# Kernel tuning notes

Measured on AMD Instinct MI355X. Metric: run time of the kernel, lower is better.

## Reference

```python
import jax, jax.numpy as jnp
import numpy as np

NUM_CLASSES = 81
THRESH_HI = 0.5
THRESH_LO = 0.4
GAMMA = 2.0
ALPHA = 0.25
VARIANCE = (0.1, 0.2)  # cfg['variance'] in ssd.pytorch
B, P, T = 32, 24564, 20


def setup_inputs() -> dict:
    key = jax.random.key(0)
    k1, k2, k3, k4, k5, k6, k7 = jax.random.split(key, 7)
    loc_data = jax.random.normal(k1, (B, P, 4), jnp.float32)
    conf_data = jax.random.normal(k2, (B, P, NUM_CLASSES), jnp.float32)
    # priors in center form (cx, cy, w, h), all in [0,1]
    pcxy = jax.random.uniform(k3, (P, 2), minval=0.05, maxval=0.95)
    pwh = jax.random.uniform(k4, (P, 2), minval=0.04, maxval=0.5)
    priors = jnp.concatenate([pcxy, pwh], axis=-1).astype(jnp.float32)
    # ground-truth boxes in point form (xmin, ymin, xmax, ymax) + label
    tcxy = jax.random.uniform(k5, (B, T, 2), minval=0.1, maxval=0.9)
    twh = jax.random.uniform(k6, (B, T, 2), minval=0.05, maxval=0.4)
    boxes = jnp.clip(jnp.concatenate([tcxy - twh / 2, tcxy + twh / 2], -1), 0.0, 1.0)
    labels = jax.random.randint(k7, (B, T), 0, NUM_CLASSES - 1).astype(jnp.float32)
    targets = jnp.concatenate([boxes, labels[..., None]], axis=-1)  # [B,T,5]
    return {"loc_data": loc_data, "conf_data": conf_data, "priors": priors, "targets": targets}


def point_form(pr):
    # center form -> (xmin,ymin,xmax,ymax)
    return jnp.concatenate([pr[:, :2] - pr[:, 2:] / 2, pr[:, :2] + pr[:, 2:] / 2], -1)


def jaccard(box_a, box_b):
    # box_a [T,4], box_b [P,4], both point form -> IoU [T,P]
    lt = jnp.maximum(box_a[:, None, :2], box_b[None, :, :2])
    rb = jnp.minimum(box_a[:, None, 2:], box_b[None, :, 2:])
    wh = jnp.clip(rb - lt, 0.0)
    inter = wh[..., 0] * wh[..., 1]
    area_a = ((box_a[:, 2] - box_a[:, 0]) * (box_a[:, 3] - box_a[:, 1]))[:, None]
    area_b = ((box_b[:, 2] - box_b[:, 0]) * (box_b[:, 3] - box_b[:, 1]))[None, :]
    return inter / (area_a + area_b - inter)


def encode(matched, priors):
    # matched [P,4] point form, priors [P,4] center form
    g_cxcy = ((matched[:, :2] + matched[:, 2:]) / 2 - priors[:, :2]) / (VARIANCE[0] * priors[:, 2:])
    g_wh = jnp.log((matched[:, 2:] - matched[:, :2]) / priors[:, 2:]) / VARIANCE[1]
    return jnp.concatenate([g_cxcy, g_wh], -1)


def match_one(truths, labels, priors):
    # truths [T,4] point form, labels [T], priors [P,4] center form
    ov = jaccard(truths, point_form(priors))          # [T,P]
    best_prior_idx = jnp.argmax(ov, axis=1)           # [T] best prior per gt
    best_truth_overlap = jnp.max(ov, axis=0)          # [P]
    best_truth_idx = jnp.argmax(ov, axis=0)           # [P]
    # ensure every gt box keeps its best prior
    best_truth_overlap = best_truth_overlap.at[best_prior_idx].set(2.0)
    best_truth_idx = best_truth_idx.at[best_prior_idx].set(jnp.arange(truths.shape[0]))
    matched = truths[best_truth_idx]                  # [P,4]
    conf = labels[best_truth_idx].astype(jnp.int32) + 1
    conf = jnp.where(best_truth_overlap < THRESH_HI, -1, conf)  # ignore band
    conf = jnp.where(best_truth_overlap < THRESH_LO, 0, conf)   # background
    return encode(matched, priors), conf


def reference(loc_data, conf_data, priors, targets):
    truths = targets[..., :4]
    labels = targets[..., 4]
    loc_t, conf_t = jax.vmap(lambda t, l: match_one(t, l, priors))(truths, labels)
    pos = conf_t > 0                                  # [B,P]
    # smooth L1 over positive priors (sum reduction)
    diff = loc_data - loc_t
    ad = jnp.abs(diff)
    sl1 = jnp.where(ad < 1.0, 0.5 * diff * diff, ad - 0.5)
    loss_l = jnp.sum(sl1 * pos[..., None])
    # focal loss over ALL locations (ignore conf==-1)
    logits = conf_data.reshape(-1, NUM_CLASSES)
    tgt = conf_t.reshape(-1)
    valid = tgt >= 0
    tgt_safe = jnp.where(valid, tgt, 0)
    logpt = jnp.take_along_axis(jax.nn.log_softmax(logits, -1), tgt_safe[:, None], 1)[:, 0]
    pt = jnp.exp(logpt)
    alpha_t = jnp.where(tgt > 0, ALPHA, 1.0 - ALPHA)
    fl = -alpha_t * (1.0 - pt) ** GAMMA * logpt
    loss_c = jnp.sum(jnp.where(valid, fl, 0.0))
    n = jnp.sum(pos).astype(loc_data.dtype)
    return loss_l / n, loss_c / n
```

## Files before the change

### kernel.cpp

```cpp
#include <hip/hip_runtime.h>

#define NCLS 81
#define BB 32
#define PP 24564
#define TT 20
#define BP_SEGS 8
#define BP_SEG 3072
#define KL_BLOCKS 1024
#define KL_ROWS 32
#define KL_CHUNKS ((BB * PP) / KL_ROWS)
#define KL_F4 ((KL_ROWS * NCLS) / 4)

#define GLOAD_LDS16(g, l)                                                  \
    __builtin_amdgcn_global_load_lds(                                      \
        (const __attribute__((address_space(1))) void*)(g),                \
        (__attribute__((address_space(3))) void*)(l), 16, 0, 0)

__global__ __launch_bounds__(1024)
void k_bp(const float* __restrict__ priors,
          const float* __restrict__ targets,
          unsigned long long* __restrict__ bp_part,
          unsigned long long* __restrict__ bovbt)
{
    const int seg = blockIdx.x;
    const int b = blockIdx.y;

    __shared__ float trb[TT * 5];
    __shared__ unsigned long long wred[TT][16];
    if (threadIdx.x < TT * 5) trb[threadIdx.x] = targets[b * TT * 5 + threadIdx.x];
    __syncthreads();

    float X1[3], Y1[3], X2[3], Y2[3], pa[3];
    unsigned int pkey[3];
    bool ok[3];
    #pragma unroll
    for (int j = 0; j < 3; ++j) {
        int p = seg * BP_SEG + j * 1024 + threadIdx.x;
        ok[j] = p < PP;
        float4 pr = ok[j] ? ((const float4*)priors)[p] : make_float4(1.f, 1.f, 0.f, 0.f);
        float hw = __fmul_rn(pr.z, 0.5f), hh = __fmul_rn(pr.w, 0.5f);
        X1[j] = __fsub_rn(pr.x, hw); Y1[j] = __fsub_rn(pr.y, hh);
        X2[j] = __fadd_rn(pr.x, hw); Y2[j] = __fadd_rn(pr.y, hh);
        pa[j] = __fmul_rn(__fsub_rn(X2[j], X1[j]), __fsub_rn(Y2[j], Y1[j]));
        pkey[j] = 0xFFFFFFFFu - (unsigned)p;
    }

    const int wv = threadIdx.x >> 6;
    const int lane = threadIdx.x & 63;

    unsigned long long bkey[3] = {0ull, 0ull, 0ull};

    for (int t = 0; t < TT; ++t) {
        float tx1 = trb[t * 5 + 0], ty1 = trb[t * 5 + 1];
        float tx2 = trb[t * 5 + 2], ty2 = trb[t * 5 + 3];
        float ta = __fmul_rn(__fsub_rn(tx2, tx1), __fsub_rn(ty2, ty1));

        unsigned long long best = 0ull;
        #pragma unroll
        for (int j = 0; j < 3; ++j) {
            float lx = fmaxf(tx1, X1[j]), ly = fmaxf(ty1, Y1[j]);
            float rx = fminf(tx2, X2[j]), ry = fminf(ty2, Y2[j]);
            float w = fmaxf(__fsub_rn(rx, lx), 0.0f);
            float h = fmaxf(__fsub_rn(ry, ly), 0.0f);
            float inter = __fmul_rn(w, h);
            float denom = __fsub_rn(__fadd_rn(ta, pa[j]), inter);
            float ov = __fdiv_rn(inter, denom);
            unsigned long long ovhi = (unsigned long long)__float_as_uint(ov) << 32;
            unsigned long long key = ok[j] ? (ovhi | pkey[j]) : 0ull;
            if (key > best) best = key;
            unsigned long long rowk = ovhi | (unsigned long long)(31 - t);
            if (rowk > bkey[j]) bkey[j] = rowk;
        }
        #pragma unroll
        for (int s = 32; s; s >>= 1) {
            unsigned long long o = __shfl_xor(best, s, 64);
            if (o > best) best = o;
        }
        if (lane == 0) wred[t][wv] = best;
    }

    #pragma unroll
    for (int j = 0; j < 3; ++j) {
        int p = seg * BP_SEG + j * 1024 + threadIdx.x;
        if (p < PP) bovbt[b * PP + p] = bkey[j];
    }

    __syncthreads();
    if (threadIdx.x < TT) {
        unsigned long long m = wred[threadIdx.x][0];
        #pragma unroll
        for (int w = 1; w < 16; ++w) if (wred[threadIdx.x][w] > m) m = wred[threadIdx.x][w];
        bp_part[(b * TT + threadIdx.x) * BP_SEGS + seg] = m;
    }
}

__global__ __launch_bounds__(64)
void k_fold(const unsigned long long* __restrict__ bp_part,
            unsigned long long* __restrict__ bovbt)
{
    int b = threadIdx.x;
    if (b < BB) {
        for (int t = 0; t < TT; ++t) {
            const unsigned long long* q = bp_part + (b * TT + t) * BP_SEGS;
            unsigned long long m = q[0];
            #pragma unroll
            for (int s = 1; s < BP_SEGS; ++s) if (q[s] > m) m = q[s];
            unsigned p = 0xFFFFFFFFu - (unsigned)(m & 0xFFFFFFFFull);
            bovbt[(size_t)b * PP + p] =
                (0x40000000ull << 32) | (unsigned long long)(31 - t);
        }
    }
}

__global__ __launch_bounds__(256, 4)
void k_stream(const float* __restrict__ conf,
              const float* __restrict__ loc,
              const float* __restrict__ priors,
              const float* __restrict__ targets,
              const unsigned long long* __restrict__ bovbt,
              float* __restrict__ pl, float* __restrict__ pn, float* __restrict__ pc)
{
    __shared__ float buf[2][KL_ROWS * NCLS];
    __shared__ float trbAll[BB * TT * 5];
    __shared__ float seb[256], xtb[256];
    __shared__ int sidx[8];
    __shared__ float red[256];

    const int tid = threadIdx.x;
    const int w = tid >> 6;
    const int lane = tid & 63;
    const int rl = tid >> 3;
    const int k = tid & 7;
    const float4* conf4 = (const float4*)conf;

    auto stage = [&](int c, int bi) {
        const float4* src = conf4 + (size_t)c * KL_F4;
        float4* dst = (float4*)buf[bi];
        #pragma unroll
        for (int j = 0; j < 2; ++j) {
            int idx = j * 256 + w * 64 + lane;
            GLOAD_LDS16(src + idx, dst + idx);
        }
        if (tid < KL_F4 - 512) {
            int idx = 512 + tid;
            GLOAD_LDS16(src + idx, dst + idx);
        }
    };

    for (int i = tid; i < BB * TT * 5; i += 256) trbAll[i] = targets[i];

    const int c0 = blockIdx.x;
    stage(c0, 0);
    __syncthreads();

    float accL = 0.0f, accN = 0.0f, accC = 0.0f;
    int cur = 0, na = 0;

    auto burst = [&](int n) {
        int span = tid >> 5;
        if (span < n) {
            int r = sidx[span] * KL_ROWS + (tid & 31);
            int b = r / PP;
            int p = r - b * PP;
            const float* trb = &trbAll[b * TT * 5];
            unsigned long long rk = bovbt[r];
            int bt = 31 - (int)(rk & 31ull);
            float bov = __uint_as_float((unsigned)(rk >> 32));
            int cc = (int)trb[bt * 5 + 4] + 1;
            if (bov < 0.5f) cc = -1;
            if (bov < 0.4f) cc = 0;
            int si = span * 32 + (tid & 31);
            if (cc > 0) {
                float4 pr = *(const float4*)(priors + p * 4);
                float mx1 = trb[bt * 5 + 0], my1 = trb[bt * 5 + 1];
                float mx2 = trb[bt * 5 + 2], my2 = trb[bt * 5 + 3];
                float cx = __fmul_rn(__fadd_rn(mx1, mx2), 0.5f);
                float cy = __fmul_rn(__fadd_rn(my1, my2), 0.5f);
                float gx = __fdiv_rn(__fsub_rn(cx, pr.x), __fmul_rn(0.1f, pr.z));
                float gy = __fdiv_rn(__fsub_rn(cy, pr.y), __fmul_rn(0.1f, pr.w));
                float gw = __fdiv_rn(logf(__fdiv_rn(__fsub_rn(mx2, mx1), pr.z)), 0.2f);
                float gh = __fdiv_rn(logf(__fdiv_rn(__fsub_rn(my2, my1), pr.w)), 0.2f);
                float4 ld = *(const float4*)(loc + (size_t)r * 4);
                float g0 = ld.x - gx, g1 = ld.y - gy, g2 = ld.z - gw, g3 = ld.w - gh;
                float a0 = fabsf(g0), a1 = fabsf(g1), a2 = fabsf(g2), a3 = fabsf(g3);
                accL += (a0 < 1.0f) ? 0.5f * g0 * g0 : (a0 - 0.5f);
                accL += (a1 < 1.0f) ? 0.5f * g1 * g1 : (a1 - 0.5f);
                accL += (a2 < 1.0f) ? 0.5f * g2 * g2 : (a2 - 0.5f);
                accL += (a3 < 1.0f) ? 0.5f * g3 * g3 : (a3 - 0.5f);
                accN += 1.0f;
            }
            if (cc >= 0) {
                float logpt = xtb[si] - __logf(seb[si]);
                float pt = __expf(logpt);
                float at = (cc > 0) ? 0.25f : 0.75f;
                float om = 1.0f - pt;
                accC -= at * om * om * logpt;
            }
        }
        __syncthreads();
    };

    for (int c = c0; c < KL_CHUNKS; c += KL_BLOCKS) {
        int cn = c + KL_BLOCKS;
        if (cn < KL_CHUNKS) stage(cn, cur ^ 1);

        int r = c * KL_ROWS + rl;
        unsigned long long rk = (k == 0) ? bovbt[r] : 0ull;

        const float* row = buf[cur] + rl * NCLS;
        float se = 0.0f;
        #pragma unroll
        for (int i = 0; i < 10; ++i) se += __expf(row[k * 10 + i]);
        if (k == 0) se += __expf(row[80]);
        se += __shfl_xor(se, 1, 8);
        se += __shfl_xor(se, 2, 8);
        se += __shfl_xor(se, 4, 8);

        if (k == 0) {
            int b = r / PP;
            int bt = 31 - (int)(rk & 31ull);
            float bov = __uint_as_float((unsigned)(rk >> 32));
            int cc = (int)trbAll[b * TT * 5 + bt * 5 + 4] + 1;
            if (bov < 0.5f) cc = -1;
            if (bov < 0.4f) cc = 0;
            seb[na * 32 + rl] = se;
            xtb[na * 32 + rl] = row[cc < 0 ? 0 : cc];
        }
        if (tid == 0) sidx[na] = c;
        __syncthreads();
        ++na;
        if (na == 8) { burst(8); na = 0; }
        cur ^= 1;
    }
    if (na > 0) burst(na);

    red[tid] = accL;
    __syncthreads();
    for (int s = 128; s; s >>= 1) {
        if (tid < s) red[tid] += red[tid + s];
        __syncthreads();
    }
    if (tid == 0) pl[blockIdx.x] = red[0];
    __syncthreads();

    red[tid] = accN;
    __syncthreads();
    for (int s = 128; s; s >>= 1) {
        if (tid < s) red[tid] += red[tid + s];
        __syncthreads();
    }
    if (tid == 0) pn[blockIdx.x] = red[0];
    __syncthreads();

    red[tid] = accC;
    __syncthreads();
    for (int s = 128; s; s >>= 1) {
        if (tid < s) red[tid] += red[tid + s];
        __syncthreads();
    }
    if (tid == 0) pc[blockIdx.x] = red[0];
}

__global__ __launch_bounds__(256)
void k_final(const float* __restrict__ pl, const float* __restrict__ pn,
             const float* __restrict__ pc, float* __restrict__ out)
{
    __shared__ float sl[256], sc[256], sn[256];
    float L = 0.0f, C = 0.0f, N = 0.0f;
    for (int i = threadIdx.x; i < KL_BLOCKS; i += 256) {
        L += pl[i]; N += pn[i]; C += pc[i];
    }
    sl[threadIdx.x] = L; sc[threadIdx.x] = C; sn[threadIdx.x] = N;
    __syncthreads();
    for (int s = 128; s; s >>= 1) {
        if (threadIdx.x < s) {
            sl[threadIdx.x] += sl[threadIdx.x + s];
            sc[threadIdx.x] += sc[threadIdx.x + s];
            sn[threadIdx.x] += sn[threadIdx.x + s];
        }
        __syncthreads();
    }
    if (threadIdx.x == 0) {
        out[0] = sl[0] / sn[0];
        out[1] = sc[0] / sn[0];
    }
}

extern "C" void kernel_launch(void* const* d_in, const int* in_sizes, int n_in,
                              void* d_out, int out_size, void* d_ws, size_t ws_size,
                              hipStream_t stream)
{
    const float* loc     = (const float*)d_in[0];
    const float* conf    = (const float*)d_in[1];
    const float* priors  = (const float*)d_in[2];
    const float* targets = (const float*)d_in[3];
    float* out = (float*)d_out;

    char* ws = (char*)d_ws;
    unsigned long long* bp_part = (unsigned long long*)ws;
    unsigned long long* bovbt   = (unsigned long long*)(ws + 65536);
    float* pl = (float*)(ws + 65536 + 6291456);
    float* pn = pl + KL_BLOCKS;
    float* pc = pn + KL_BLOCKS;

    k_bp<<<dim3(BP_SEGS, BB), 1024, 0, stream>>>(priors, targets, bp_part, bovbt);
    k_fold<<<1, 64, 0, stream>>>(bp_part, bovbt);
    k_stream<<<KL_BLOCKS, 256, 0, stream>>>(conf, loc, priors, targets, bovbt,
                                            pl, pn, pc);
    k_final<<<1, 256, 0, stream>>>(pl, pn, pc, out);
}
```

Measured before the change: 81.26 us.

## Replace syncthreads with partial vmcnt waits to overlap conf staging

The double-buffered global-to-LDS staging loop now uses explicit s_waitcnt vmcnt(N) with raw s_barrier, so the next chunk's loads stay in flight while the current chunk is processed, instead of __syncthreads draining all memory ops. The bovbt load is also prefetched one iteration ahead, and staging is repartitioned so each wave copies a contiguous 162-float4 slice. The barrier at the end of burst is removed. This relies on a hand-counted vmcnt, and a wrong count or a missing barrier could cause LDS races.

```diff
diff --git a/kernel.cpp b/kernel.cpp
--- a/kernel.cpp
+++ b/kernel.cpp
@@ -134,25 +134,16 @@
     const float4* conf4 = (const float4*)conf;
 
     auto stage = [&](int c, int bi) {
-        const float4* src = conf4 + (size_t)c * KL_F4;
-        float4* dst = (float4*)buf[bi];
-        #pragma unroll
-        for (int j = 0; j < 2; ++j) {
-            int idx = j * 256 + w * 64 + lane;
-            GLOAD_LDS16(src + idx, dst + idx);
-        }
-        if (tid < KL_F4 - 512) {
-            int idx = 512 + tid;
-            GLOAD_LDS16(src + idx, dst + idx);
-        }
+        const float4* src = conf4 + (size_t)c * KL_F4 + w * 162;
+        float4* dst = (float4*)buf[bi] + w * 162;
+        GLOAD_LDS16(src + lane, dst + lane);
+        GLOAD_LDS16(src + 64 + lane, dst + 64 + lane);
+        if (lane < 34) GLOAD_LDS16(src + 128 + lane, dst + 128 + lane);
     };
 
     for (int i = tid; i < BB * TT * 5; i += 256) trbAll[i] = targets[i];
 
     const int c0 = blockIdx.x;
-    stage(c0, 0);
-    __syncthreads();
-
     float accL = 0.0f, accN = 0.0f, accC = 0.0f;
     int cur = 0, na = 0;
 
@@ -197,15 +188,26 @@
                 accC -= at * om * om * logpt;
             }
         }
-        __syncthreads();
     };
 
+    unsigned long long rk = 0ull;
+    stage(c0, 0);
+    if (k == 0) rk = bovbt[c0 * KL_ROWS + rl];
+
     for (int c = c0; c < KL_CHUNKS; c += KL_BLOCKS) {
-        int cn = c + KL_BLOCKS;
-        if (cn < KL_CHUNKS) stage(cn, cur ^ 1);
-
-        int r = c * KL_ROWS + rl;
-        unsigned long long rk = (k == 0) ? bovbt[r] : 0ull;
+        const int cn = c + KL_BLOCKS;
+        const bool hasnext = cn < KL_CHUNKS;
+        unsigned long long rkn = 0ull;
+        if (hasnext) {
+            stage(cn, cur ^ 1);
+            if (k == 0) rkn = bovbt[cn * KL_ROWS + rl];
+        }
+
+        __builtin_amdgcn_sched_barrier(0);
+        if (hasnext) asm volatile("s_waitcnt vmcnt(4) lgkmcnt(0)" ::: "memory");
+        else         asm volatile("s_waitcnt vmcnt(0) lgkmcnt(0)" ::: "memory");
+        __builtin_amdgcn_s_barrier();
+        __builtin_amdgcn_sched_barrier(0);
 
         const float* row = buf[cur] + rl * NCLS;
         float se = 0.0f;
@@ -217,6 +219,7 @@
         se += __shfl_xor(se, 4, 8);
 
         if (k == 0) {
+            int r = c * KL_ROWS + rl;
             int b = r / PP;
             int bt = 31 - (int)(rk & 31ull);
             float bov = __uint_as_float((unsigned)(rk >> 32));
@@ -227,12 +230,19 @@
             xtb[na * 32 + rl] = row[cc < 0 ? 0 : cc];
         }
         if (tid == 0) sidx[na] = c;
-        __syncthreads();
+
+        __builtin_amdgcn_sched_barrier(0);
+        asm volatile("s_waitcnt lgkmcnt(0)" ::: "memory");
+        __builtin_amdgcn_s_barrier();
+        __builtin_amdgcn_sched_barrier(0);
+
         ++na;
         if (na == 8) { burst(8); na = 0; }
+        rk = rkn;
         cur ^= 1;
     }
     if (na > 0) burst(na);
+    __syncthreads();
 
     red[tid] = accL;
     __syncthreads();
```

After: 81.59 us. About the same (+0.4%).

## Replace fold kernel with atomicMax and apply best-prior override in stream kernel

Applied to the files above, without the earlier changes.

Removes the single-block k_fold launch. Per-segment best-prior keys are now reduced with global atomicMax into a zeroed buffer, and each k_stream block loads the final best-prior indices into LDS. The forced-match override then happens in the burst phase through a 20-way compare per row. The target-class logit is no longer captured from LDS during the streaming loop; it is read from global conf inside the burst. This trades a launch and a serial kernel for an extra memset, atomics, per-row compare loops, and scattered global reads of conf.

```diff
diff --git a/kernel.cpp b/kernel.cpp
--- a/kernel.cpp
+++ b/kernel.cpp
@@ -19,7 +19,7 @@
 __global__ __launch_bounds__(1024)
 void k_bp(const float* __restrict__ priors,
           const float* __restrict__ targets,
-          unsigned long long* __restrict__ bp_part,
+          unsigned long long* __restrict__ bp_final,
           unsigned long long* __restrict__ bovbt)
 {
     const int seg = blockIdx.x;
@@ -90,25 +90,7 @@
         unsigned long long m = wred[threadIdx.x][0];
         #pragma unroll
         for (int w = 1; w < 16; ++w) if (wred[threadIdx.x][w] > m) m = wred[threadIdx.x][w];
-        bp_part[(b * TT + threadIdx.x) * BP_SEGS + seg] = m;
-    }
-}
-
-__global__ __launch_bounds__(64)
-void k_fold(const unsigned long long* __restrict__ bp_part,
-            unsigned long long* __restrict__ bovbt)
-{
-    int b = threadIdx.x;
-    if (b < BB) {
-        for (int t = 0; t < TT; ++t) {
-            const unsigned long long* q = bp_part + (b * TT + t) * BP_SEGS;
-            unsigned long long m = q[0];
-            #pragma unroll
-            for (int s = 1; s < BP_SEGS; ++s) if (q[s] > m) m = q[s];
-            unsigned p = 0xFFFFFFFFu - (unsigned)(m & 0xFFFFFFFFull);
-            bovbt[(size_t)b * PP + p] =
-                (0x40000000ull << 32) | (unsigned long long)(31 - t);
-        }
+        atomicMax(&bp_final[b * TT + threadIdx.x], m);
     }
 }
 
@@ -117,12 +99,14 @@
               const float* __restrict__ loc,
               const float* __restrict__ priors,
               const float* __restrict__ targets,
+              const unsigned long long* __restrict__ bp_final,
               const unsigned long long* __restrict__ bovbt,
               float* __restrict__ pl, float* __restrict__ pn, float* __restrict__ pc)
 {
     __shared__ float buf[2][KL_ROWS * NCLS];
     __shared__ float trbAll[BB * TT * 5];
-    __shared__ float seb[256], xtb[256];
+    __shared__ unsigned int bpAll[BB * TT];
+    __shared__ float seb[256];
     __shared__ int sidx[8];
     __shared__ float red[256];
 
@@ -148,6 +132,8 @@
     };
 
     for (int i = tid; i < BB * TT * 5; i += 256) trbAll[i] = targets[i];
+    for (int i = tid; i < BB * TT; i += 256)
+        bpAll[i] = 0xFFFFFFFFu - (unsigned)(bp_final[i] & 0xFFFFFFFFull);
 
     const int c0 = blockIdx.x;
     stage(c0, 0);
@@ -163,13 +149,21 @@
             int b = r / PP;
             int p = r - b * PP;
             const float* trb = &trbAll[b * TT * 5];
+            const unsigned int* bpb = &bpAll[b * TT];
+
             unsigned long long rk = bovbt[r];
             int bt = 31 - (int)(rk & 31ull);
             float bov = __uint_as_float((unsigned)(rk >> 32));
+            int ft = -1;
+            #pragma unroll
+            for (int t = 0; t < TT; ++t) {
+                if (bpb[t] == (unsigned)p) ft = t;
+            }
+            if (ft >= 0) { bt = ft; bov = 2.0f; }
             int cc = (int)trb[bt * 5 + 4] + 1;
             if (bov < 0.5f) cc = -1;
             if (bov < 0.4f) cc = 0;
-            int si = span * 32 + (tid & 31);
+
             if (cc > 0) {
                 float4 pr = *(const float4*)(priors + p * 4);
                 float mx1 = trb[bt * 5 + 0], my1 = trb[bt * 5 + 1];
@@ -190,7 +184,8 @@
                 accN += 1.0f;
             }
             if (cc >= 0) {
-                float logpt = xtb[si] - __logf(seb[si]);
+                float xt = conf[(size_t)r * NCLS + cc];
+                float logpt = xt - __logf(seb[span * 32 + (tid & 31)]);
                 float pt = __expf(logpt);
                 float at = (cc > 0) ? 0.25f : 0.75f;
                 float om = 1.0f - pt;
@@ -204,9 +199,6 @@
         int cn = c + KL_BLOCKS;
         if (cn < KL_CHUNKS) stage(cn, cur ^ 1);
 
-        int r = c * KL_ROWS + rl;
-        unsigned long long rk = (k == 0) ? bovbt[r] : 0ull;
-
         const float* row = buf[cur] + rl * NCLS;
         float se = 0.0f;
         #pragma unroll
@@ -216,16 +208,7 @@
         se += __shfl_xor(se, 2, 8);
         se += __shfl_xor(se, 4, 8);
 
-        if (k == 0) {
-            int b = r / PP;
-            int bt = 31 - (int)(rk & 31ull);
-            float bov = __uint_as_float((unsigned)(rk >> 32));
-            int cc = (int)trbAll[b * TT * 5 + bt * 5 + 4] + 1;
-            if (bov < 0.5f) cc = -1;
-            if (bov < 0.4f) cc = 0;
-            seb[na * 32 + rl] = se;
-            xtb[na * 32 + rl] = row[cc < 0 ? 0 : cc];
-        }
+        if (k == 0) seb[na * 32 + rl] = se;
         if (tid == 0) sidx[na] = c;
         __syncthreads();
         ++na;
@@ -297,15 +280,15 @@
     float* out = (float*)d_out;
 
     char* ws = (char*)d_ws;
-    unsigned long long* bp_part = (unsigned long long*)ws;
-    unsigned long long* bovbt   = (unsigned long long*)(ws + 65536);
+    unsigned long long* bp_final = (unsigned long long*)ws;
+    unsigned long long* bovbt    = (unsigned long long*)(ws + 65536);
     float* pl = (float*)(ws + 65536 + 6291456);
     float* pn = pl + KL_BLOCKS;
     float* pc = pn + KL_BLOCKS;
 
-    k_bp<<<dim3(BP_SEGS, BB), 1024, 0, stream>>>(priors, targets, bp_part, bovbt);
-    k_fold<<<1, 64, 0, stream>>>(bp_part, bovbt);
-    k_stream<<<KL_BLOCKS, 256, 0, stream>>>(conf, loc, priors, targets, bovbt,
-                                            pl, pn, pc);
+    hipMemsetAsync(bp_final, 0, BB * TT * sizeof(unsigned long long), stream);
+    k_bp<<<dim3(BP_SEGS, BB), 1024, 0, stream>>>(priors, targets, bp_final, bovbt);
+    k_stream<<<KL_BLOCKS, 256, 0, stream>>>(conf, loc, priors, targets, bp_final,
+                                            bovbt, pl, pn, pc);
     k_final<<<1, 256, 0, stream>>>(pl, pn, pc, out);
 }
```

After: 88.73 us. +9.2%, slower.
